# Kernel tuning notes

Hardware: AMD Instinct MI355X
Metric: run time of the kernel (lower is better)

## Reference

```python
import jax, jax.numpy as jnp
import numpy as np

D = 1024
NH = 16
HD = D // NH
DFF = 4 * D
EPS = 1e-5


def setup_inputs() -> dict:
    key = jax.random.key(0)
    ks = jax.random.split(key, 12)
    s = lambda fan_in: 1.0 / np.sqrt(fan_in)
    return {
        "x": jax.random.normal(ks[0], (2, 2048, D), dtype=jnp.float32),
        # weights stored [in, out] (transpose of torch Linear layout)
        "w_qkv": jax.random.uniform(ks[1], (D, 3 * D), minval=-s(D), maxval=s(D)),
        "w_proj": jax.random.uniform(ks[2], (D, D), minval=-s(D), maxval=s(D)),
        "ln1_w": jnp.ones((D,), jnp.float32),
        "ln1_b": jnp.zeros((D,), jnp.float32),
        "ln2_w": jnp.ones((D,), jnp.float32),
        "ln2_b": jnp.zeros((D,), jnp.float32),
        "fc1_w": jax.random.uniform(ks[3], (D, DFF), minval=-s(D), maxval=s(D)),
        "fc1_b": jax.random.uniform(ks[4], (DFF,), minval=-s(D), maxval=s(D)),
        "fc2_w": jax.random.uniform(ks[5], (DFF, D), minval=-s(DFF), maxval=s(DFF)),
        "fc2_b": jax.random.uniform(ks[6], (D,), minval=-s(DFF), maxval=s(DFF)),
    }


def _layernorm(x, w, b):
    mu = jnp.mean(x, axis=-1, keepdims=True)
    var = jnp.mean(jnp.square(x - mu), axis=-1, keepdims=True)
    return (x - mu) * jax.lax.rsqrt(var + EPS) * w + b


def _attn(x, w_qkv, w_proj):
    B, T, C = x.shape
    qkv = x @ w_qkv  # [B,T,3C]
    q, k, v = jnp.split(qkv, 3, axis=-1)
    q = q.reshape(B, T, NH, HD).transpose(0, 2, 1, 3)  # [B,nh,T,hd]
    k = k.reshape(B, T, NH, HD).transpose(0, 2, 1, 3)
    v = v.reshape(B, T, NH, HD).transpose(0, 2, 1, 3)
    att = jnp.einsum("bhqd,bhkd->bhqk", q, k) / np.sqrt(HD)
    causal = jnp.tril(jnp.ones((T, T), bool))
    att = jnp.where(causal, att, -jnp.inf)
    att = jax.nn.softmax(att, axis=-1)
    out = jnp.einsum("bhqk,bhkd->bhqd", att, v)
    out = out.transpose(0, 2, 1, 3).reshape(B, T, C)
    return out @ w_proj


def reference(x, w_qkv, w_proj, ln1_w, ln1_b, ln2_w, ln2_b, fc1_w, fc1_b, fc2_w, fc2_b):
    x = x + _attn(_layernorm(x, ln1_w, ln1_b), w_qkv, w_proj)
    h = _layernorm(x, ln2_w, ln2_b)
    h = jax.nn.gelu(h @ fc1_w + fc1_b, approximate=False) @ fc2_w + fc2_b
    return x + h
```

## Files before the change

### kernel.cpp

```cpp
#include <hip/hip_runtime.h>


typedef short  bf16x8 __attribute__((ext_vector_type(8)));
typedef short  bf16x4 __attribute__((ext_vector_type(4)));
typedef float  fx4    __attribute__((ext_vector_type(4)));

#define DEV static __device__ __forceinline__

DEV short f2bf(float f) {
    unsigned u = __builtin_bit_cast(unsigned, f);
    u += 0x7fffu + ((u >> 16) & 1u);
    return (short)(u >> 16);
}

template <int CTRL> DEV float dppmax(float v) {
    int x = __builtin_amdgcn_update_dpp(0, __builtin_bit_cast(int, v), CTRL, 0xF, 0xF, true);
    return fmaxf(v, __builtin_bit_cast(float, x));
}
template <int CTRL> DEV float dppadd(float v) {
    int x = __builtin_amdgcn_update_dpp(0, __builtin_bit_cast(int, v), CTRL, 0xF, 0xF, true);
    return v + __builtin_bit_cast(float, x);
}
DEV float rowmax16(float v) {
    v = dppmax<0x121>(v); v = dppmax<0x122>(v); v = dppmax<0x124>(v); v = dppmax<0x128>(v);
    return v;
}
DEV float rowsum16(float v) {
    v = dppadd<0x121>(v); v = dppadd<0x122>(v); v = dppadd<0x124>(v); v = dppadd<0x128>(v);
    return v;
}

#define AS1(p) ((__attribute__((address_space(1))) void*)(p))
#define AS3(p) ((__attribute__((address_space(3))) void*)(p))

__global__ __launch_bounds__(256) void ln_kernel(const float* __restrict__ x,
                                                 const float* __restrict__ w,
                                                 const float* __restrict__ b,
                                                 short* __restrict__ out)
{
    int row = blockIdx.x;
    int tid = threadIdx.x;
    const float4 v = *(const float4*)(x + (size_t)row * 1024 + tid * 4);
    float s = v.x + v.y + v.z + v.w;
    float q = v.x * v.x + v.y * v.y + v.z * v.z + v.w * v.w;
#pragma unroll
    for (int off = 32; off > 0; off >>= 1) {
        s += __shfl_down(s, off);
        q += __shfl_down(q, off);
    }
    __shared__ float ls[4], lq[4];
    if ((tid & 63) == 0) { ls[tid >> 6] = s; lq[tid >> 6] = q; }
    __syncthreads();
    float S  = ls[0] + ls[1] + ls[2] + ls[3];
    float Q  = lq[0] + lq[1] + lq[2] + lq[3];
    float mu  = S * (1.0f / 1024.0f);
    float var = Q * (1.0f / 1024.0f) - mu * mu;
    float inv = rsqrtf(var + 1e-5f);
    float4 wv = *(const float4*)(w + tid * 4);
    float4 bv = *(const float4*)(b + tid * 4);
    bf16x4 o;
    o[0] = f2bf((v.x - mu) * inv * wv.x + bv.x);
    o[1] = f2bf((v.y - mu) * inv * wv.y + bv.y);
    o[2] = f2bf((v.z - mu) * inv * wv.z + bv.z);
    o[3] = f2bf((v.w - mu) * inv * wv.w + bv.w);
    *(bf16x4*)(out + (size_t)row * 1024 + tid * 4) = o;
}

__global__ void transpose_f32_bf16(const float* __restrict__ in,
                                   short* __restrict__ out, int R, int C)
{
    __shared__ float tile[32][33];
    int c0 = blockIdx.x * 32, r0 = blockIdx.y * 32;
    int tx = threadIdx.x, ty = threadIdx.y;
#pragma unroll
    for (int dy = 0; dy < 32; dy += 8)
        tile[ty + dy][tx] = in[(size_t)(r0 + ty + dy) * C + c0 + tx];
    __syncthreads();
#pragma unroll
    for (int dy = 0; dy < 32; dy += 8)
        out[(size_t)(c0 + ty + dy) * R + r0 + tx] = f2bf(tile[tx][ty + dy]);
}

__global__ void vt_extract(const short* __restrict__ qkv, short* __restrict__ vt)
{
    __shared__ short tile[32][33];
    int t0 = blockIdx.x * 32, d0 = blockIdx.y * 32;
    int bh = blockIdx.z;
    int tx = threadIdx.x, ty = threadIdx.y;
    size_t inbase  = (size_t)(bh >> 4) * 2048 * 3072 + 2048 + (bh & 15) * 64;
    size_t outbase = (size_t)bh * 64 * 2048;
#pragma unroll
    for (int dy = 0; dy < 32; dy += 8)
        tile[ty + dy][tx] = qkv[inbase + (size_t)(t0 + ty + dy) * 3072 + d0 + tx];
    __syncthreads();
#pragma unroll
    for (int dy = 0; dy < 32; dy += 8)
        vt[outbase + (size_t)(d0 + ty + dy) * 2048 + t0 + tx] = tile[tx][ty + dy];
}

template <int BN, bool BIAS, bool GELU, bool RESID, bool OUT_BF16, bool PARTIAL>
__global__ __launch_bounds__(256) void gemm_bt(const short* __restrict__ A,
                                               const short* __restrict__ Bt,
                                               void* __restrict__ Cout,
                                               void* __restrict__ Cout2,
                                               const float* __restrict__ bias,
                                               const float* __restrict__ resid,
                                               int M, int N, int K)
{
    constexpr int NJ = BN / 32;
    __shared__ short As[2][128 * 32];
    __shared__ short Bs[2][BN * 32];
    int tid  = threadIdx.x;
    int lane = tid & 63, wv = tid >> 6;
    int quad = lane >> 4, l15 = lane & 15;
    int m0 = blockIdx.y * 128, n0 = blockIdx.x * BN;
    int SK   = gridDim.z;
    int kbeg = blockIdx.z * (K / SK);
    int NK   = (K / SK) / 32;
    int wr = (wv >> 1) * 64, wc = (wv & 1) * (BN / 2);
    fx4 acc[4][NJ] = {};
    int srow = lane >> 2;
    int scol = ((lane & 3) ^ (srow & 3)) * 8;
    int rg   = (quad ^ (l15 & 3)) * 8;
    const short* Ab = A  + (size_t)m0 * K;
    const short* Bb = Bt + (size_t)n0 * K;

    auto stage = [&](int buf, int k0) {
#pragma unroll
        for (int c = wv; c < 8; c += 4) {
            int row = c * 16 + srow;
            __builtin_amdgcn_global_load_lds(AS1(Ab + (size_t)row * K + k0 + scol),
                                             AS3(&As[buf][c * 512]), 16, 0, 0);
        }
#pragma unroll
        for (int c = wv; c < BN / 16; c += 4) {
            int row = c * 16 + srow;
            __builtin_amdgcn_global_load_lds(AS1(Bb + (size_t)row * K + k0 + scol),
                                             AS3(&Bs[buf][c * 512]), 16, 0, 0);
        }
    };

    stage(0, kbeg);
    __syncthreads();
    for (int kt = 0; kt < NK; ++kt) {
        int cur = kt & 1;
        if (kt + 1 < NK) stage(cur ^ 1, kbeg + (kt + 1) * 32);
        bf16x8 af[4], bfr[NJ];
#pragma unroll
        for (int i = 0; i < 4; ++i)
            af[i] = *(const bf16x8*)&As[cur][(wr + i * 16 + l15) * 32 + rg];
#pragma unroll
        for (int j = 0; j < NJ; ++j)
            bfr[j] = *(const bf16x8*)&Bs[cur][(wc + j * 16 + l15) * 32 + rg];
#pragma unroll
        for (int i = 0; i < 4; ++i)
#pragma unroll
            for (int j = 0; j < NJ; ++j)
                acc[i][j] = __builtin_amdgcn_mfma_f32_16x16x32_bf16(af[i], bfr[j], acc[i][j], 0, 0, 0);
        __syncthreads();
    }

    if constexpr (PARTIAL) {
        float* P = blockIdx.z ? (float*)Cout2 : (float*)Cout;
#pragma unroll
        for (int i = 0; i < 4; ++i)
#pragma unroll
            for (int j = 0; j < NJ; ++j)
#pragma unroll
                for (int r = 0; r < 4; ++r) {
                    int row = m0 + wr + i * 16 + quad * 4 + r;
                    int col = n0 + wc + j * 16 + l15;
                    P[(size_t)row * N + col] = acc[i][j][r];
                }
    } else {
#pragma unroll
        for (int i = 0; i < 4; ++i)
#pragma unroll
            for (int j = 0; j < NJ; ++j)
#pragma unroll
                for (int r = 0; r < 4; ++r) {
                    int row = m0 + wr + i * 16 + quad * 4 + r;
                    int col = n0 + wc + j * 16 + l15;
                    float v = acc[i][j][r];
                    if constexpr (BIAS)  v += bias[col];
                    if constexpr (GELU)  v = 0.5f * v * (1.0f + erff(v * 0.70710678118654752f));
                    if constexpr (RESID) v += resid[(size_t)row * N + col];
                    if constexpr (OUT_BF16) ((short*)Cout)[(size_t)row * N + col] = f2bf(v);
                    else                    ((float*)Cout)[(size_t)row * N + col] = v;
                }
    }
}

template <bool BIAS>
__global__ __launch_bounds__(256) void reduce2(const float* __restrict__ p0,
                                               const float* __restrict__ p1,
                                               const float* __restrict__ resid,
                                               const float* __restrict__ bias,
                                               float* __restrict__ out, int N)
{
    size_t idx = ((size_t)blockIdx.x * 256 + threadIdx.x) * 4;
    float4 a = *(const float4*)(p0 + idx);
    float4 b = *(const float4*)(p1 + idx);
    float4 r = *(const float4*)(resid + idx);
    float4 v;
    v.x = a.x + b.x + r.x; v.y = a.y + b.y + r.y;
    v.z = a.z + b.z + r.z; v.w = a.w + b.w + r.w;
    if constexpr (BIAS) {
        const float4 bv = *(const float4*)(bias + (idx & (N - 1)));
        v.x += bv.x; v.y += bv.y; v.z += bv.z; v.w += bv.w;
    }
    *(float4*)(out + idx) = v;
}

__global__ __launch_bounds__(256) void attn_kernel(const short* __restrict__ qkv,
                                                   const short* __restrict__ vt,
                                                   short* __restrict__ out)
{
    __shared__ short Ks[2][64 * 64];
    __shared__ short Vs[2][64 * 64];
    __shared__ short Ps[4 * 16 * 64];
    const float CS = 0.125f * 1.44269504088896f;
    int tid  = threadIdx.x, lane = tid & 63, wv = tid >> 6;
    int quad = lane >> 4, l15 = lane & 15;
    int b = blockIdx.z, h = blockIdx.y, j = blockIdx.x;

    const size_t kbase = (size_t)b * 2048 * 3072 + 1024 + h * 64;
    const size_t vbase = (size_t)(b * 16 + h) * 64 * 2048;
    int srow = lane >> 3;
    int sg   = lane & 7;
    int scol = (sg ^ srow) * 8;
    int rg0  = (quad ^ (l15 & 7)) * 8;

    for (int item = 0; item < 2; ++item) {
        int qt = item ? j : 31 - j;
        int q0 = qt * 64;

        bf16x8 qf[2];
#pragma unroll
        for (int ks = 0; ks < 2; ++ks)
            qf[ks] = *(const bf16x8*)&qkv[(size_t)(b * 2048 + q0 + wv * 16 + l15) * 3072
                                           + h * 64 + ks * 32 + quad * 8];
        float mi[4], li[4];
        fx4 oacc[4] = {};
#pragma unroll
        for (int r = 0; r < 4; ++r) { mi[r] = -1e30f; li[r] = 0.0f; }

#pragma unroll
        for (int c = wv; c < 8; c += 4) {
            int row = c * 8 + srow;
            __builtin_amdgcn_global_load_lds(AS1(qkv + kbase + (size_t)row * 3072 + scol),
                                             AS3(&Ks[0][c * 512]), 16, 0, 0);
            __builtin_amdgcn_global_load_lds(AS1(vt + vbase + (size_t)row * 2048 + scol),
                                             AS3(&Vs[0][c * 512]), 16, 0, 0);
        }
        __syncthreads();

        for (int kt = 0; kt <= qt; ++kt) {
            int cur = kt & 1;
            if (kt < qt) {
                int nb = cur ^ 1;
                int tn = (kt + 1) * 64;
#pragma unroll
                for (int c = wv; c < 8; c += 4) {
                    int row = c * 8 + srow;
                    __builtin_amdgcn_global_load_lds(AS1(qkv + kbase + (size_t)(tn + row) * 3072 + scol),
                                                     AS3(&Ks[nb][c * 512]), 16, 0, 0);
                    __builtin_amdgcn_global_load_lds(AS1(vt + vbase + (size_t)row * 2048 + tn + scol),
                                                     AS3(&Vs[nb][c * 512]), 16, 0, 0);
                }
            }

            fx4 s[4];
#pragma unroll
            for (int nt = 0; nt < 4; ++nt) {
                bf16x8 kf0 = *(const bf16x8*)&Ks[cur][(nt * 16 + l15) * 64 + rg0];
                bf16x8 kf1 = *(const bf16x8*)&Ks[cur][(nt * 16 + l15) * 64 + (rg0 ^ 32)];
                fx4 z = {0.f, 0.f, 0.f, 0.f};
                z = __builtin_amdgcn_mfma_f32_16x16x32_bf16(qf[0], kf0, z, 0, 0, 0);
                z = __builtin_amdgcn_mfma_f32_16x16x32_bf16(qf[1], kf1, z, 0, 0, 0);
                s[nt] = z;
            }
            if (kt == qt) {
#pragma unroll
                for (int nt = 0; nt < 4; ++nt)
#pragma unroll
                    for (int r = 0; r < 4; ++r)
                        if (nt * 16 + l15 > wv * 16 + quad * 4 + r) s[nt][r] = -1e30f;
            }

            float mnew[4], alpha[4], rsum[4];
#pragma unroll
            for (int r = 0; r < 4; ++r) {
                float v = fmaxf(fmaxf(s[0][r], s[1][r]), fmaxf(s[2][r], s[3][r]));
                v = rowmax16(v);
                mnew[r]  = fmaxf(mi[r], v);
                alpha[r] = exp2f((mi[r] - mnew[r]) * CS);
                mi[r] = mnew[r];
                rsum[r] = 0.0f;
            }
#pragma unroll
            for (int nt = 0; nt < 4; ++nt)
#pragma unroll
                for (int r = 0; r < 4; ++r) {
                    float p = exp2f((s[nt][r] - mnew[r]) * CS);
                    rsum[r] += p;
                    int rr = quad * 4 + r;
                    int col = nt * 16 + l15;
                    int g = (col >> 3) ^ (rr & 7);
                    Ps[wv * 1024 + rr * 64 + g * 8 + (col & 7)] = f2bf(p);
                }
#pragma unroll
            for (int r = 0; r < 4; ++r) {
                float v = rowsum16(rsum[r]);
                li[r] = li[r] * alpha[r] + v;
#pragma unroll
                for (int dt = 0; dt < 4; ++dt) oacc[dt][r] *= alpha[r];
            }

            bf16x8 pf0 = *(const bf16x8*)&Ps[wv * 1024 + l15 * 64 + rg0];
            bf16x8 pf1 = *(const bf16x8*)&Ps[wv * 1024 + l15 * 64 + (rg0 ^ 32)];
#pragma unroll
            for (int dt = 0; dt < 4; ++dt) {
                bf16x8 vf0 = *(const bf16x8*)&Vs[cur][(dt * 16 + l15) * 64 + rg0];
                bf16x8 vf1 = *(const bf16x8*)&Vs[cur][(dt * 16 + l15) * 64 + (rg0 ^ 32)];
                oacc[dt] = __builtin_amdgcn_mfma_f32_16x16x32_bf16(pf0, vf0, oacc[dt], 0, 0, 0);
                oacc[dt] = __builtin_amdgcn_mfma_f32_16x16x32_bf16(pf1, vf1, oacc[dt], 0, 0, 0);
            }
            __syncthreads();
        }

        float inv[4];
#pragma unroll
        for (int r = 0; r < 4; ++r) inv[r] = 1.0f / li[r];
#pragma unroll
        for (int dt = 0; dt < 4; ++dt)
#pragma unroll
            for (int r = 0; r < 4; ++r) {
                int row = q0 + wv * 16 + quad * 4 + r;
                int col = h * 64 + dt * 16 + l15;
                out[((size_t)b * 2048 + row) * 1024 + col] = f2bf(oacc[dt][r] * inv[r]);
            }
    }
}

extern "C" void kernel_launch(void* const* d_in, const int* in_sizes, int n_in,
                              void* d_out, int out_size, void* d_ws, size_t ws_size,
                              hipStream_t stream)
{
    const float* x      = (const float*)d_in[0];
    const float* w_qkv  = (const float*)d_in[1];
    const float* w_proj = (const float*)d_in[2];
    const float* ln1_w  = (const float*)d_in[3];
    const float* ln1_b  = (const float*)d_in[4];
    const float* ln2_w  = (const float*)d_in[5];
    const float* ln2_b  = (const float*)d_in[6];
    const float* fc1_w  = (const float*)d_in[7];
    const float* fc1_b  = (const float*)d_in[8];
    const float* fc2_w  = (const float*)d_in[9];
    const float* fc2_b  = (const float*)d_in[10];
    float* out = (float*)d_out;
    char*  ws  = (char*)d_ws;

    size_t off = 0;
    auto alloc = [&](size_t bytes) { void* p = ws + off; off += (bytes + 255) & ~(size_t)255; return p; };
    short* tw_qkv  = (short*)alloc((size_t)3072 * 1024 * 2);
    short* tw_proj = (short*)alloc((size_t)1024 * 1024 * 2);
    short* tfc1    = (short*)alloc((size_t)4096 * 1024 * 2);
    short* tfc2    = (short*)alloc((size_t)1024 * 4096 * 2);
    short* xn      = (short*)alloc((size_t)4096 * 1024 * 2);
    short* qkvb    = (short*)alloc((size_t)4096 * 3072 * 2);
    short* vtb     = (short*)alloc((size_t)32 * 64 * 2048 * 2);
    short* attnb   = (short*)alloc((size_t)4096 * 1024 * 2);
    float* x1      = (float*)alloc((size_t)4096 * 1024 * 4);
    float* pk      = (float*)alloc((size_t)4096 * 1024 * 4);
    short* h1      = qkvb;

    dim3 tb(32, 8);
    transpose_f32_bf16<<<dim3(3072 / 32, 1024 / 32), tb, 0, stream>>>(w_qkv, tw_qkv, 1024, 3072);
    transpose_f32_bf16<<<dim3(1024 / 32, 1024 / 32), tb, 0, stream>>>(w_proj, tw_proj, 1024, 1024);
    transpose_f32_bf16<<<dim3(4096 / 32, 1024 / 32), tb, 0, stream>>>(fc1_w, tfc1, 1024, 4096);
    transpose_f32_bf16<<<dim3(1024 / 32, 4096 / 32), tb, 0, stream>>>(fc2_w, tfc2, 4096, 1024);

    ln_kernel<<<4096, 256, 0, stream>>>(x, ln1_w, ln1_b, xn);
    gemm_bt<128, false, false, false, true, false><<<dim3(24, 32, 1), 256, 0, stream>>>(
        xn, tw_qkv, qkvb, nullptr, nullptr, nullptr, 4096, 3072, 1024);
    vt_extract<<<dim3(2048 / 32, 64 / 32, 32), tb, 0, stream>>>(qkvb, vtb);
    attn_kernel<<<dim3(16, 16, 2), 256, 0, stream>>>(qkvb, vtb, attnb);
    gemm_bt<64, false, false, false, false, true><<<dim3(16, 32, 2), 256, 0, stream>>>(
        attnb, tw_proj, x1, pk, nullptr, nullptr, 4096, 1024, 1024);
    reduce2<false><<<4096, 256, 0, stream>>>(x1, pk, x, nullptr, x1, 1024);
    ln_kernel<<<4096, 256, 0, stream>>>(x1, ln2_w, ln2_b, xn);
    gemm_bt<128, true, true, false, true, false><<<dim3(32, 32, 1), 256, 0, stream>>>(
        xn, tfc1, h1, nullptr, fc1_b, nullptr, 4096, 4096, 1024);
    gemm_bt<64, false, false, false, false, true><<<dim3(16, 32, 2), 256, 0, stream>>>(
        h1, tfc2, out, pk, nullptr, nullptr, 4096, 1024, 4096);
    reduce2<true><<<4096, 256, 0, stream>>>(out, pk, x1, fc2_b, out, 1024);
}
```

Before: 397.5 us.

## Keep softmax probabilities in registers via transposed QK MFMA in attention

The attention kernel now computes S^T (K as the A operand), so each lane holds one query row's scores. The probabilities can then be packed straight into bf16 registers and fed to 16x16x16 MFMAs for PV, with no round trip through the Ps LDS buffer. Row max and sum become two cross-lane shuffles instead of DPP chains, and alpha and l are broadcast back with shuffles. The grid also changes from paired causal tiles (two per block) to one q-tile per block with heavy tiles launched first. This trades load balancing within a block for more blocks and less LDS use.

```diff
diff --git a/kernel.cpp b/kernel.cpp
--- a/kernel.cpp
+++ b/kernel.cpp
@@ -4,6 +4,7 @@
 typedef short  bf16x8 __attribute__((ext_vector_type(8)));
 typedef short  bf16x4 __attribute__((ext_vector_type(4)));
 typedef float  fx4    __attribute__((ext_vector_type(4)));
+typedef int    ix2    __attribute__((ext_vector_type(2)));
 
 #define DEV static __device__ __forceinline__
 
@@ -11,23 +12,6 @@
     unsigned u = __builtin_bit_cast(unsigned, f);
     u += 0x7fffu + ((u >> 16) & 1u);
     return (short)(u >> 16);
-}
-
-template <int CTRL> DEV float dppmax(float v) {
-    int x = __builtin_amdgcn_update_dpp(0, __builtin_bit_cast(int, v), CTRL, 0xF, 0xF, true);
-    return fmaxf(v, __builtin_bit_cast(float, x));
-}
-template <int CTRL> DEV float dppadd(float v) {
-    int x = __builtin_amdgcn_update_dpp(0, __builtin_bit_cast(int, v), CTRL, 0xF, 0xF, true);
-    return v + __builtin_bit_cast(float, x);
-}
-DEV float rowmax16(float v) {
-    v = dppmax<0x121>(v); v = dppmax<0x122>(v); v = dppmax<0x124>(v); v = dppmax<0x128>(v);
-    return v;
-}
-DEV float rowsum16(float v) {
-    v = dppadd<0x121>(v); v = dppadd<0x122>(v); v = dppadd<0x124>(v); v = dppadd<0x128>(v);
-    return v;
 }
 
 #define AS1(p) ((__attribute__((address_space(1))) void*)(p))
@@ -218,129 +202,138 @@
 {
     __shared__ short Ks[2][64 * 64];
     __shared__ short Vs[2][64 * 64];
-    __shared__ short Ps[4 * 16 * 64];
     const float CS = 0.125f * 1.44269504088896f;
     int tid  = threadIdx.x, lane = tid & 63, wv = tid >> 6;
     int quad = lane >> 4, l15 = lane & 15;
-    int b = blockIdx.z, h = blockIdx.y, j = blockIdx.x;
+    int b = blockIdx.z, h = blockIdx.y;
+    int qt = 31 - blockIdx.x;
+    int q0 = qt * 64;
 
     const size_t kbase = (size_t)b * 2048 * 3072 + 1024 + h * 64;
     const size_t vbase = (size_t)(b * 16 + h) * 64 * 2048;
     int srow = lane >> 3;
-    int sg   = lane & 7;
-    int scol = (sg ^ srow) * 8;
+    int scol = ((lane & 7) ^ srow) * 8;
     int rg0  = (quad ^ (l15 & 7)) * 8;
 
-    for (int item = 0; item < 2; ++item) {
-        int qt = item ? j : 31 - j;
-        int q0 = qt * 64;
-
-        bf16x8 qf[2];
-#pragma unroll
-        for (int ks = 0; ks < 2; ++ks)
-            qf[ks] = *(const bf16x8*)&qkv[(size_t)(b * 2048 + q0 + wv * 16 + l15) * 3072
-                                           + h * 64 + ks * 32 + quad * 8];
-        float mi[4], li[4];
-        fx4 oacc[4] = {};
-#pragma unroll
-        for (int r = 0; r < 4; ++r) { mi[r] = -1e30f; li[r] = 0.0f; }
-
-#pragma unroll
-        for (int c = wv; c < 8; c += 4) {
-            int row = c * 8 + srow;
-            __builtin_amdgcn_global_load_lds(AS1(qkv + kbase + (size_t)row * 3072 + scol),
-                                             AS3(&Ks[0][c * 512]), 16, 0, 0);
-            __builtin_amdgcn_global_load_lds(AS1(vt + vbase + (size_t)row * 2048 + scol),
-                                             AS3(&Vs[0][c * 512]), 16, 0, 0);
+    bf16x8 qf[2];
+#pragma unroll
+    for (int ks = 0; ks < 2; ++ks)
+        qf[ks] = *(const bf16x8*)&qkv[(size_t)(b * 2048 + q0 + wv * 16 + l15) * 3072
+                                       + h * 64 + ks * 32 + quad * 8];
+    float mi = -3e38f, li = 0.0f;
+    fx4 oacc[4] = {};
+
+#pragma unroll
+    for (int c = wv; c < 8; c += 4) {
+        int row = c * 8 + srow;
+        __builtin_amdgcn_global_load_lds(AS1(qkv + kbase + (size_t)row * 3072 + scol),
+                                         AS3(&Ks[0][c * 512]), 16, 0, 0);
+        __builtin_amdgcn_global_load_lds(AS1(vt + vbase + (size_t)row * 2048 + scol),
+                                         AS3(&Vs[0][c * 512]), 16, 0, 0);
+    }
+    __syncthreads();
+
+    for (int kt = 0; kt <= qt; ++kt) {
+        int cur = kt & 1;
+        if (kt < qt) {
+            int nb = cur ^ 1, tn = (kt + 1) * 64;
+#pragma unroll
+            for (int c = wv; c < 8; c += 4) {
+                int row = c * 8 + srow;
+                __builtin_amdgcn_global_load_lds(AS1(qkv + kbase + (size_t)(tn + row) * 3072 + scol),
+                                                 AS3(&Ks[nb][c * 512]), 16, 0, 0);
+                __builtin_amdgcn_global_load_lds(AS1(vt + vbase + (size_t)row * 2048 + tn + scol),
+                                                 AS3(&Vs[nb][c * 512]), 16, 0, 0);
+            }
+        }
+
+        fx4 s[4];
+#pragma unroll
+        for (int nt = 0; nt < 4; ++nt) {
+            bf16x8 kf0 = *(const bf16x8*)&Ks[cur][(nt * 16 + l15) * 64 + rg0];
+            bf16x8 kf1 = *(const bf16x8*)&Ks[cur][(nt * 16 + l15) * 64 + (rg0 ^ 32)];
+            fx4 z = {0.f, 0.f, 0.f, 0.f};
+            z = __builtin_amdgcn_mfma_f32_16x16x32_bf16(kf0, qf[0], z, 0, 0, 0);
+            z = __builtin_amdgcn_mfma_f32_16x16x32_bf16(kf1, qf[1], z, 0, 0, 0);
+            s[nt] = z;
+        }
+        if (kt == qt) {
+            int qrow = wv * 16 + l15;
+#pragma unroll
+            for (int nt = 0; nt < 4; ++nt)
+#pragma unroll
+                for (int r = 0; r < 4; ++r)
+                    if (nt * 16 + quad * 4 + r > qrow) s[nt][r] = -3e38f;
+        }
+
+        float m0_ = fmaxf(fmaxf(s[0][0], s[0][1]), fmaxf(s[0][2], s[0][3]));
+        float m1_ = fmaxf(fmaxf(s[1][0], s[1][1]), fmaxf(s[1][2], s[1][3]));
+        float m2_ = fmaxf(fmaxf(s[2][0], s[2][1]), fmaxf(s[2][2], s[2][3]));
+        float m3_ = fmaxf(fmaxf(s[3][0], s[3][1]), fmaxf(s[3][2], s[3][3]));
+        float vmax = fmaxf(fmaxf(m0_, m1_), fmaxf(m2_, m3_));
+        vmax = fmaxf(vmax, __shfl_xor(vmax, 16));
+        vmax = fmaxf(vmax, __shfl_xor(vmax, 32));
+        float mnew  = fmaxf(mi, vmax);
+        float alpha = exp2f((mi - mnew) * CS);
+        float mc    = mnew * CS;
+        mi = mnew;
+
+        bf16x4 pf[4];
+        float rs = 0.0f;
+#pragma unroll
+        for (int nt = 0; nt < 4; ++nt) {
+            float p0 = exp2f(fmaf(s[nt][0], CS, -mc));
+            float p1 = exp2f(fmaf(s[nt][1], CS, -mc));
+            float p2 = exp2f(fmaf(s[nt][2], CS, -mc));
+            float p3 = exp2f(fmaf(s[nt][3], CS, -mc));
+            rs += (p0 + p1) + (p2 + p3);
+            unsigned a0 = __builtin_bit_cast(unsigned, p0) + 0x8000u;
+            unsigned a1 = __builtin_bit_cast(unsigned, p1) + 0x8000u;
+            unsigned a2 = __builtin_bit_cast(unsigned, p2) + 0x8000u;
+            unsigned a3 = __builtin_bit_cast(unsigned, p3) + 0x8000u;
+            ix2 pk;
+            pk[0] = (int)__builtin_amdgcn_perm(a1, a0, 0x07060302u);
+            pk[1] = (int)__builtin_amdgcn_perm(a3, a2, 0x07060302u);
+            pf[nt] = __builtin_bit_cast(bf16x4, pk);
+        }
+        rs += __shfl_xor(rs, 16);
+        rs += __shfl_xor(rs, 32);
+        li = li * alpha + rs;
+
+        float arow[4];
+#pragma unroll
+        for (int r = 0; r < 4; ++r) arow[r] = __shfl(alpha, quad * 4 + r, 16);
+#pragma unroll
+        for (int dt = 0; dt < 4; ++dt)
+#pragma unroll
+            for (int r = 0; r < 4; ++r) oacc[dt][r] *= arow[r];
+
+#pragma unroll
+        for (int dt = 0; dt < 4; ++dt) {
+            int vrow  = dt * 16 + l15;
+            int rbase = vrow * 64 + (quad & 1) * 4;
+            int rk    = vrow & 7;
+#pragma unroll
+            for (int nt = 0; nt < 4; ++nt) {
+                int g = (nt * 2 + (quad >> 1)) ^ rk;
+                bf16x4 vf = *(const bf16x4*)&Vs[cur][rbase + g * 8];
+                oacc[dt] = __builtin_amdgcn_mfma_f32_16x16x16bf16_1k(pf[nt], vf, oacc[dt], 0, 0, 0);
+            }
         }
         __syncthreads();
-
-        for (int kt = 0; kt <= qt; ++kt) {
-            int cur = kt & 1;
-            if (kt < qt) {
-                int nb = cur ^ 1;
-                int tn = (kt + 1) * 64;
-#pragma unroll
-                for (int c = wv; c < 8; c += 4) {
-                    int row = c * 8 + srow;
-                    __builtin_amdgcn_global_load_lds(AS1(qkv + kbase + (size_t)(tn + row) * 3072 + scol),
-                                                     AS3(&Ks[nb][c * 512]), 16, 0, 0);
-                    __builtin_amdgcn_global_load_lds(AS1(vt + vbase + (size_t)row * 2048 + tn + scol),
-                                                     AS3(&Vs[nb][c * 512]), 16, 0, 0);
-                }
-            }
-
-            fx4 s[4];
-#pragma unroll
-            for (int nt = 0; nt < 4; ++nt) {
-                bf16x8 kf0 = *(const bf16x8*)&Ks[cur][(nt * 16 + l15) * 64 + rg0];
-                bf16x8 kf1 = *(const bf16x8*)&Ks[cur][(nt * 16 + l15) * 64 + (rg0 ^ 32)];
-                fx4 z = {0.f, 0.f, 0.f, 0.f};
-                z = __builtin_amdgcn_mfma_f32_16x16x32_bf16(qf[0], kf0, z, 0, 0, 0);
-                z = __builtin_amdgcn_mfma_f32_16x16x32_bf16(qf[1], kf1, z, 0, 0, 0);
-                s[nt] = z;
-            }
-            if (kt == qt) {
-#pragma unroll
-                for (int nt = 0; nt < 4; ++nt)
-#pragma unroll
-                    for (int r = 0; r < 4; ++r)
-                        if (nt * 16 + l15 > wv * 16 + quad * 4 + r) s[nt][r] = -1e30f;
-            }
-
-            float mnew[4], alpha[4], rsum[4];
-#pragma unroll
-            for (int r = 0; r < 4; ++r) {
-                float v = fmaxf(fmaxf(s[0][r], s[1][r]), fmaxf(s[2][r], s[3][r]));
-                v = rowmax16(v);
-                mnew[r]  = fmaxf(mi[r], v);
-                alpha[r] = exp2f((mi[r] - mnew[r]) * CS);
-                mi[r] = mnew[r];
-                rsum[r] = 0.0f;
-            }
-#pragma unroll
-            for (int nt = 0; nt < 4; ++nt)
-#pragma unroll
-                for (int r = 0; r < 4; ++r) {
-                    float p = exp2f((s[nt][r] - mnew[r]) * CS);
-                    rsum[r] += p;
-                    int rr = quad * 4 + r;
-                    int col = nt * 16 + l15;
-                    int g = (col >> 3) ^ (rr & 7);
-                    Ps[wv * 1024 + rr * 64 + g * 8 + (col & 7)] = f2bf(p);
-                }
-#pragma unroll
-            for (int r = 0; r < 4; ++r) {
-                float v = rowsum16(rsum[r]);
-                li[r] = li[r] * alpha[r] + v;
-#pragma unroll
-                for (int dt = 0; dt < 4; ++dt) oacc[dt][r] *= alpha[r];
-            }
-
-            bf16x8 pf0 = *(const bf16x8*)&Ps[wv * 1024 + l15 * 64 + rg0];
-            bf16x8 pf1 = *(const bf16x8*)&Ps[wv * 1024 + l15 * 64 + (rg0 ^ 32)];
-#pragma unroll
-            for (int dt = 0; dt < 4; ++dt) {
-                bf16x8 vf0 = *(const bf16x8*)&Vs[cur][(dt * 16 + l15) * 64 + rg0];
-                bf16x8 vf1 = *(const bf16x8*)&Vs[cur][(dt * 16 + l15) * 64 + (rg0 ^ 32)];
-                oacc[dt] = __builtin_amdgcn_mfma_f32_16x16x32_bf16(pf0, vf0, oacc[dt], 0, 0, 0);
-                oacc[dt] = __builtin_amdgcn_mfma_f32_16x16x32_bf16(pf1, vf1, oacc[dt], 0, 0, 0);
-            }
-            __syncthreads();
-        }
-
-        float inv[4];
-#pragma unroll
-        for (int r = 0; r < 4; ++r) inv[r] = 1.0f / li[r];
-#pragma unroll
-        for (int dt = 0; dt < 4; ++dt)
-#pragma unroll
-            for (int r = 0; r < 4; ++r) {
-                int row = q0 + wv * 16 + quad * 4 + r;
-                int col = h * 64 + dt * 16 + l15;
-                out[((size_t)b * 2048 + row) * 1024 + col] = f2bf(oacc[dt][r] * inv[r]);
-            }
-    }
+    }
+
+    float linv[4];
+#pragma unroll
+    for (int r = 0; r < 4; ++r) linv[r] = 1.0f / __shfl(li, quad * 4 + r, 16);
+#pragma unroll
+    for (int dt = 0; dt < 4; ++dt)
+#pragma unroll
+        for (int r = 0; r < 4; ++r) {
+            int row = q0 + wv * 16 + quad * 4 + r;
+            int col = h * 64 + dt * 16 + l15;
+            out[((size_t)b * 2048 + row) * 1024 + col] = f2bf(oacc[dt][r] * linv[r]);
+        }
 }
 
 extern "C" void kernel_launch(void* const* d_in, const int* in_sizes, int n_in,
@@ -385,7 +378,7 @@
     gemm_bt<128, false, false, false, true, false><<<dim3(24, 32, 1), 256, 0, stream>>>(
         xn, tw_qkv, qkvb, nullptr, nullptr, nullptr, 4096, 3072, 1024);
     vt_extract<<<dim3(2048 / 32, 64 / 32, 32), tb, 0, stream>>>(qkvb, vtb);
-    attn_kernel<<<dim3(16, 16, 2), 256, 0, stream>>>(qkvb, vtb, attnb);
+    attn_kernel<<<dim3(32, 16, 2), 256, 0, stream>>>(qkvb, vtb, attnb);
     gemm_bt<64, false, false, false, false, true><<<dim3(16, 32, 2), 256, 0, stream>>>(
         attnb, tw_proj, x1, pk, nullptr, nullptr, 4096, 1024, 1024);
     reduce2<false><<<4096, 256, 0, stream>>>(x1, pk, x, nullptr, x1, 1024);
```

Measured after the change: 422.8 us. 6.4% more time.
